# Performance work log

Hardware: AMD Instinct MI355X
Metric: run time of the kernel (lower is better)

Reference implementation:

```python
import jax, jax.numpy as jnp
import numpy as np

N, F_IN, HID, HEADS, E, G, CLS = 20000, 128, 32, 8, 320000, 64, 10


def setup_inputs() -> dict:
    key = jax.random.key(0)
    ks = jax.random.split(key, 16)
    HC = HEADS * HID
    inp = {
        'x': jax.random.normal(ks[0], (N, F_IN), jnp.float32),
        'edge_index': jax.random.randint(ks[1], (2, E), 0, N, jnp.int64),
        'batch': jnp.sort(jax.random.randint(ks[2], (N,), 0, G, jnp.int64)),
        'W1': jax.random.normal(ks[3], (F_IN, HC), jnp.float32) * 0.1,
        'att_l1': jax.random.normal(ks[4], (HEADS, HID), jnp.float32) * 0.1,
        'att_r1': jax.random.normal(ks[5], (HEADS, HID), jnp.float32) * 0.1,
        'b1': jnp.zeros((HC,), jnp.float32),
        'W2': jax.random.normal(ks[6], (HC, HC), jnp.float32) * 0.1,
        'att_l2': jax.random.normal(ks[7], (HEADS, HID), jnp.float32) * 0.1,
        'att_r2': jax.random.normal(ks[8], (HEADS, HID), jnp.float32) * 0.1,
        'b2': jnp.zeros((HC,), jnp.float32),
        'lin_W': jax.random.normal(ks[9], (HC, CLS), jnp.float32) * 0.1,
        'lin_b': jnp.zeros((CLS,), jnp.float32),
    }
    return inp


def _add_self_loops(edge_index):
    loops = jnp.arange(N, dtype=edge_index.dtype)
    return (jnp.concatenate([edge_index[0], loops]),
            jnp.concatenate([edge_index[1], loops]))


def _supergat_conv(x, edge_index, W, att_l, att_r, b):
    # SuperGATConv, attention_type='MX', eval mode (no dropout / neg sampling)
    h = (x @ W).reshape(-1, HEADS, HID)          # [N, H, C]
    src, dst = _add_self_loops(edge_index)       # j -> i
    x_j = h[src]                                 # [Etot, H, C]
    x_i = h[dst]
    logits = jnp.einsum('ehc,ehc->eh', x_i, x_j)            # dot-product part
    alpha = jnp.einsum('ehc,hc->eh', x_j, att_l) + jnp.einsum('ehc,hc->eh', x_i, att_r)
    alpha = alpha * jax.nn.sigmoid(logits)
    alpha = jax.nn.leaky_relu(alpha, 0.2)
    # segment softmax over incoming edges of each dst node
    amax = jax.ops.segment_max(alpha, dst, num_segments=N)
    ex = jnp.exp(alpha - amax[dst])
    denom = jax.ops.segment_sum(ex, dst, num_segments=N)
    attn = ex / (denom[dst] + 1e-16)             # [Etot, H]
    out = jax.ops.segment_sum(x_j * attn[..., None], dst, num_segments=N)  # [N,H,C]
    return out.reshape(-1, HEADS * HID) + b


def reference(x, edge_index, batch, W1, att_l1, att_r1, b1, W2, att_l2, att_r2, b2, lin_W, lin_b):
    h = _supergat_conv(x, edge_index, W1, att_l1, att_r1, b1)
    h = jax.nn.elu(h)
    h = _supergat_conv(h, edge_index, W2, att_l2, att_r2, b2)
    # global mean pool over graphs
    sums = jax.ops.segment_sum(h, batch, num_segments=G)
    cnts = jax.ops.segment_sum(jnp.ones((h.shape[0], 1), h.dtype), batch, num_segments=G)
    pooled = sums / jnp.maximum(cnts, 1.0)
    return pooled @ lin_W + lin_b
```

## Files before the change

kernel.cpp:

```cpp
#include <hip/hip_runtime.h>
#include <hip/hip_bf16.h>
#include <math.h>

#define NNODE 20000
#define FIN   128
#define HC    256
#define HEADS 8
#define HID   32
#define NEDGE 320000
#define ETOT  (NEDGE + NNODE)
#define NGRAPH 64
#define NCLS  10
#define MAXDEG 64

typedef __attribute__((ext_vector_type(8))) short short8v;
typedef __attribute__((ext_vector_type(8))) unsigned short ushort8v;
typedef __attribute__((ext_vector_type(4))) float float4v;

__device__ __forceinline__ ushort f2bf(float f) {
    __hip_bfloat16 b = __float2bfloat16(f);
    return *(ushort*)&b;
}
__device__ __forceinline__ float bf2f(ushort u) {
    return __uint_as_float(((unsigned)u) << 16);
}


#define ZB_DEG ((NNODE + 255) / 256)
#define ZB_PS  ((NGRAPH * HC + NGRAPH + 255) / 256)

__global__ __launch_bounds__(256) void init_kernel(const float* __restrict__ W1,
                                                   const float* __restrict__ W2,
                                                   ushort* __restrict__ W1t,
                                                   ushort* __restrict__ W2t,
                                                   int* __restrict__ deg,
                                                   float* __restrict__ psum) {
    int b = blockIdx.x;
    if (b < 128) {
        int e = b * 256 + threadIdx.x;
        int k = e >> 8, n = e & 255;
        W1t[(long)n * FIN + k] = f2bf(W1[(long)k * 256 + n]);
    } else if (b < 384) {
        int e = (b - 128) * 256 + threadIdx.x;
        int k = e >> 8, n = e & 255;
        W2t[(long)n * HC + k] = f2bf(W2[(long)k * 256 + n]);
    } else if (b < 384 + ZB_DEG) {
        int i = (b - 384) * 256 + threadIdx.x;
        if (i < NNODE) deg[i] = 0;
    } else {
        int i = (b - 384 - ZB_DEG) * 256 + threadIdx.x;
        if (i < NGRAPH * HC + NGRAPH) psum[i] = 0.f;
    }
}


__global__ __launch_bounds__(256) void fill_slots(const int* __restrict__ ei,
                                                  int* __restrict__ deg,
                                                  int* __restrict__ esrc) {
    int e = blockIdx.x * blockDim.x + threadIdx.x;
    if (e >= ETOT) return;
    int src, dst;
    if (e < NEDGE) { src = ei[e]; dst = ei[NEDGE + e]; }
    else           { src = e - NEDGE; dst = src; }
    int slot = atomicAdd(&deg[dst], 1);
    if (slot < MAXDEG) esrc[dst * MAXDEG + slot] = src;
}


template<bool A_FP32>
__global__ __launch_bounds__(256) void gemm_mfma(const void* __restrict__ Aptr,
                                                 const ushort* __restrict__ Bt,
                                                 ushort* __restrict__ C,
                                                 const float* __restrict__ attL,
                                                 const float* __restrict__ attR,
                                                 float* __restrict__ aL,
                                                 float* __restrict__ aR,
                                                 int M, int K) {
    __shared__ __align__(16) ushort As[64][72];
    __shared__ __align__(16) ushort Bs[64][72];
    int tid = threadIdx.x;
    int rowBase = blockIdx.x * 64;
    int colBase = blockIdx.y * 64;
    int wave = tid >> 6;
    int l = tid & 63;
    int lm = l & 15;
    int quad = l >> 4;
    int r0 = (wave >> 1) * 32;
    int c0 = (wave & 1) * 32;

    float4v acc00 = {0.f, 0.f, 0.f, 0.f};
    float4v acc01 = acc00, acc10 = acc00, acc11 = acc00;

    for (int k0 = 0; k0 < K; k0 += 64) {
        if (A_FP32) {
            const float* A = (const float*)Aptr;
            #pragma unroll
            for (int q = 0; q < 4; q++) {
                int idx = tid + q * 256;
                int r   = idx >> 4;
                int kc  = (idx & 15) * 4;
                int grow = rowBase + r;
                float4 v = make_float4(0.f, 0.f, 0.f, 0.f);
                if (grow < M) v = *(const float4*)(A + (long)grow * K + k0 + kc);
                ushort4 o = { f2bf(v.x), f2bf(v.y), f2bf(v.z), f2bf(v.w) };
                *(ushort4*)&As[r][kc] = o;
            }
            #pragma unroll
            for (int q = 0; q < 2; q++) {
                int ch = tid + q * 256;
                int r  = ch >> 3;
                int kc = (ch & 7) * 8;
                *(short8v*)&Bs[r][kc] =
                    *(const short8v*)(Bt + (long)(colBase + r) * K + k0 + kc);
            }
        } else {
            const ushort* A = (const ushort*)Aptr;
            #pragma unroll
            for (int q = 0; q < 2; q++) {
                int ch = tid + q * 256;
                int r  = ch >> 3;
                int kc = (ch & 7) * 8;
                int grow = rowBase + r;
                short8v av = {};
                if (grow < M) av = *(const short8v*)(A + (long)grow * K + k0 + kc);
                *(short8v*)&As[r][kc] = av;
                *(short8v*)&Bs[r][kc] =
                    *(const short8v*)(Bt + (long)(colBase + r) * K + k0 + kc);
            }
        }
        __syncthreads();
        #pragma unroll
        for (int ks = 0; ks < 64; ks += 32) {
            int kb = ks + quad * 8;
            short8v a0 = *(const short8v*)&As[r0 + lm][kb];
            short8v a1 = *(const short8v*)&As[r0 + 16 + lm][kb];
            short8v b0 = *(const short8v*)&Bs[c0 + lm][kb];
            short8v b1 = *(const short8v*)&Bs[c0 + 16 + lm][kb];
            acc00 = __builtin_amdgcn_mfma_f32_16x16x32_bf16(a0, b0, acc00, 0, 0, 0);
            acc01 = __builtin_amdgcn_mfma_f32_16x16x32_bf16(a0, b1, acc01, 0, 0, 0);
            acc10 = __builtin_amdgcn_mfma_f32_16x16x32_bf16(a1, b0, acc10, 0, 0, 0);
            acc11 = __builtin_amdgcn_mfma_f32_16x16x32_bf16(a1, b1, acc11, 0, 0, 0);
        }
        __syncthreads();
    }

    int cb = colBase + c0;
    int hd = cb >> 5;
    float al0 = attL[cb + lm], al1 = attL[cb + 16 + lm];
    float ar0 = attR[cb + lm], ar1 = attR[cb + 16 + lm];
    #pragma unroll
    for (int mi = 0; mi < 2; mi++) {
        float4v s0 = mi ? acc10 : acc00;
        float4v s1 = mi ? acc11 : acc01;
        #pragma unroll
        for (int r = 0; r < 4; r++) {
            int row = rowBase + r0 + mi * 16 + quad * 4 + r;
            float pl = s0[r] * al0 + s1[r] * al1;
            float pr = s0[r] * ar0 + s1[r] * ar1;
            #pragma unroll
            for (int s2 = 1; s2 < 16; s2 <<= 1) {
                pl += __shfl_xor(pl, s2);
                pr += __shfl_xor(pr, s2);
            }
            if (row < M) {
                C[(long)row * 256 + cb + lm]      = f2bf(s0[r]);
                C[(long)row * 256 + cb + 16 + lm] = f2bf(s1[r]);
                if (lm == 0) {
                    aL[row * 8 + hd] = pl;
                    aR[row * 8 + hd] = pr;
                }
            }
        }
    }
}


__global__ __launch_bounds__(256) void fused_attn(const ushort* __restrict__ h,
                                                  const int* __restrict__ degv,
                                                  const int* __restrict__ esrc,
                                                  const float* __restrict__ aL,
                                                  const float* __restrict__ aR,
                                                  const float* __restrict__ bias,
                                                  ushort* __restrict__ out,
                                                  int apply_elu) {
    int wave = threadIdx.x >> 6;
    int node = blockIdx.x * 4 + wave;
    if (node >= NNODE) return;
    int l = threadIdx.x & 63;
    int slot = l >> 5;
    int lh = l & 31;
    int head = lh >> 2;

    const ushort8v* h8 = (const ushort8v*)h;
    ushort8v hiu = h8[(long)node * 32 + lh];
    float hi[8];
    #pragma unroll
    for (int c = 0; c < 8; c++) hi[c] = bf2f(hiu[c]);
    float a_ri = aR[node * 8 + head];
    int beg = node * MAXDEG;
    int deg = min(degv[node], MAXDEG);

    float lsum = 0.f;
    float acc[8] = {0.f, 0.f, 0.f, 0.f, 0.f, 0.f, 0.f, 0.f};

    int p = slot;
    int j0 = (p < deg) ? esrc[beg + p] : 0;
    ushort8v hjA = h8[(long)j0 * 32 + lh];
    float alA = aL[j0 * 8 + head];
    int j1 = (p + 2 < deg) ? esrc[beg + p + 2] : 0;

    for (; p < deg; p += 2) {
        ushort8v hjB = h8[(long)j1 * 32 + lh];
        float alB = aL[j1 * 8 + head];
        int j2 = (p + 4 < deg) ? esrc[beg + p + 4] : 0;

        float hj[8];
        #pragma unroll
        for (int c = 0; c < 8; c++) hj[c] = bf2f(hjA[c]);
        float prod = hi[0] * hj[0];
        #pragma unroll
        for (int c = 1; c < 8; c++) prod += hi[c] * hj[c];
        prod += __shfl_xor(prod, 1);
        prod += __shfl_xor(prod, 2);
        float alpha = (alA + a_ri) * __builtin_amdgcn_rcpf(1.f + __expf(-prod));
        alpha = (alpha > 0.f) ? alpha : 0.2f * alpha;
        float ex = __expf(alpha);
        lsum += ex;
        #pragma unroll
        for (int c = 0; c < 8; c++) acc[c] += ex * hj[c];

        hjA = hjB; alA = alB; j1 = j2;
    }

    lsum += __shfl_xor(lsum, 32);
    #pragma unroll
    for (int c = 0; c < 8; c++) acc[c] += __shfl_xor(acc[c], 32);

    if (slot == 0) {
        float inv = __builtin_amdgcn_rcpf(lsum + 1e-16f);
        float4 b0 = ((const float4*)bias)[lh * 2];
        float4 b1 = ((const float4*)bias)[lh * 2 + 1];
        float bb[8] = {b0.x, b0.y, b0.z, b0.w, b1.x, b1.y, b1.z, b1.w};
        ushort8v o;
        #pragma unroll
        for (int c = 0; c < 8; c++) {
            float r = acc[c] * inv + bb[c];
            if (apply_elu) r = (r > 0.f) ? r : (__expf(r) - 1.f);
            o[c] = f2bf(r);
        }
        *(ushort8v*)(out + (long)node * 256 + lh * 8) = o;
    }
}


__global__ __launch_bounds__(256) void pool_kernel(const ushort* __restrict__ h,
                                                   const int* __restrict__ batch,
                                                   float* __restrict__ psum,
                                                   float* __restrict__ pcnt) {
    int t = threadIdx.x;
    int n0 = blockIdx.x * 64;
    int n1 = min(n0 + 64, NNODE);
    if (n0 >= NNODE) return;
    float accv = 0.f;
    int gcur = batch[n0];
    for (int n = n0; n < n1; ++n) {
        int g = batch[n];
        if (g != gcur) {
            atomicAdd(&psum[gcur * HC + t], accv);
            accv = 0.f;
            gcur = g;
        }
        accv += bf2f(h[(long)n * HC + t]);
    }
    atomicAdd(&psum[gcur * HC + t], accv);
    if (t == 0) {
        int cnt = 0;
        int gc = batch[n0];
        for (int n = n0; n < n1; ++n) {
            int g = batch[n];
            if (g != gc) { atomicAdd(&pcnt[gc], (float)cnt); cnt = 0; gc = g; }
            cnt++;
        }
        atomicAdd(&pcnt[gc], (float)cnt);
    }
}

__global__ void final_kernel(const float* __restrict__ psum, const float* __restrict__ pcnt,
                             const float* __restrict__ linW, const float* __restrict__ linb,
                             float* __restrict__ out) {
    int g = blockIdx.x;
    int t = threadIdx.x;
    __shared__ float p[HC];
    float c = fmaxf(pcnt[g], 1.f);
    p[t] = psum[g * HC + t] / c;
    __syncthreads();
    if (t < NCLS) {
        float s = linb[t];
        for (int cch = 0; cch < HC; cch++) s += p[cch] * linW[cch * NCLS + t];
        out[g * NCLS + t] = s;
    }
}


extern "C" void kernel_launch(void* const* d_in, const int* in_sizes, int n_in,
                              void* d_out, int out_size, void* d_ws, size_t ws_size,
                              hipStream_t stream) {
    const float* x     = (const float*)d_in[0];
    const int*   ei    = (const int*)d_in[1];
    const int*   batch = (const int*)d_in[2];
    const float* W1    = (const float*)d_in[3];
    const float* attL1 = (const float*)d_in[4];
    const float* attR1 = (const float*)d_in[5];
    const float* b1    = (const float*)d_in[6];
    const float* W2    = (const float*)d_in[7];
    const float* attL2 = (const float*)d_in[8];
    const float* attR2 = (const float*)d_in[9];
    const float* b2    = (const float*)d_in[10];
    const float* linW  = (const float*)d_in[11];
    const float* linb  = (const float*)d_in[12];
    float* out = (float*)d_out;

    char* w = (char*)d_ws;
    size_t o = 0;
    int* deg    = (int*)(w + o); o += (size_t)NNODE * 4;
    o = (o + 15) & ~(size_t)15;
    int* esrc   = (int*)(w + o); o += (size_t)NNODE * MAXDEG * 4;
    o = (o + 15) & ~(size_t)15;
    ushort* W1t = (ushort*)(w + o); o += (size_t)FIN * HC * 2;
    ushort* W2t = (ushort*)(w + o); o += (size_t)HC * HC * 2;
    o = (o + 15) & ~(size_t)15;
    ushort* hbA = (ushort*)(w + o); o += (size_t)NNODE * HC * 2;
    ushort* hbB = (ushort*)(w + o); o += (size_t)NNODE * HC * 2;
    o = (o + 15) & ~(size_t)15;
    float* aL   = (float*)(w + o); o += (size_t)NNODE * HEADS * 4;
    float* aR   = (float*)(w + o); o += (size_t)NNODE * HEADS * 4;
    float* psum = (float*)(w + o); o += (size_t)NGRAPH * HC * 4;
    float* pcnt = (float*)(w + o); o += (size_t)NGRAPH * 4;

    init_kernel<<<384 + ZB_DEG + ZB_PS, 256, 0, stream>>>(W1, W2, W1t, W2t, deg, psum);

    int eb = (ETOT + 255) / 256;
    fill_slots<<<eb, 256, 0, stream>>>(ei, deg, esrc);

    dim3 gg((NNODE + 63) / 64, HC / 64);
    int ab = (NNODE + 3) / 4;
    gemm_mfma<true><<<gg, 256, 0, stream>>>(x, W1t, hbA, attL1, attR1, aL, aR, NNODE, FIN);
    fused_attn<<<ab, 256, 0, stream>>>(hbA, deg, esrc, aL, aR, b1, hbB, 1);
    gemm_mfma<false><<<gg, 256, 0, stream>>>(hbB, W2t, hbA, attL2, attR2, aL, aR, NNODE, HC);
    fused_attn<<<ab, 256, 0, stream>>>(hbA, deg, esrc, aL, aR, b2, hbB, 0);
    pool_kernel<<<(NNODE + 63) / 64, 256, 0, stream>>>(hbB, batch, psum, pcnt);
    final_kernel<<<NGRAPH, 256, 0, stream>>>(psum, pcnt, linW, linb, out);
}
```

Before: 221.1 us.

## Merge all stages into one cooperative persistent kernel with grid syncs

Replaces the eight separate kernel launches with a single cooperative kernel. It loops over work items with grid-stride loops and uses grid.sync() between the init, edge-fill, GEMM, attention, pooling and final phases. The aim is to remove launch overhead and inter-kernel gaps. In exchange the grid is capped at 1024 blocks, so phases such as attention (5000 blocks' worth of work) and the GEMM lose oversubscription. Grid-wide barriers and a host occupancy query on every call add their own cost.

```diff
diff --git a/kernel.cpp b/kernel.cpp
--- a/kernel.cpp
+++ b/kernel.cpp
@@ -1,6 +1,9 @@
 #include <hip/hip_runtime.h>
+#include <hip/hip_cooperative_groups.h>
 #include <hip/hip_bf16.h>
 #include <math.h>
+
+namespace cg = cooperative_groups;
 
 #define NNODE 20000
 #define FIN   128
@@ -13,6 +16,12 @@
 #define NCLS  10
 #define MAXDEG 64
 
+#define ZB_DEG ((NNODE + 255) / 256)
+#define ZB_PS  ((NGRAPH * HC + NGRAPH + 255) / 256)
+#define GEMM_TILES (((NNODE + 63) / 64) * 4)
+#define ATTN_Q ((NNODE + 3) / 4)
+#define POOL_B ((NNODE + 63) / 64)
+
 typedef __attribute__((ext_vector_type(8))) short short8v;
 typedef __attribute__((ext_vector_type(8))) unsigned short ushort8v;
 typedef __attribute__((ext_vector_type(4))) float float4v;
@@ -25,62 +34,29 @@
     return __uint_as_float(((unsigned)u) << 16);
 }
 
-
-#define ZB_DEG ((NNODE + 255) / 256)
-#define ZB_PS  ((NGRAPH * HC + NGRAPH + 255) / 256)
-
-__global__ __launch_bounds__(256) void init_kernel(const float* __restrict__ W1,
-                                                   const float* __restrict__ W2,
-                                                   ushort* __restrict__ W1t,
-                                                   ushort* __restrict__ W2t,
-                                                   int* __restrict__ deg,
-                                                   float* __restrict__ psum) {
-    int b = blockIdx.x;
-    if (b < 128) {
-        int e = b * 256 + threadIdx.x;
-        int k = e >> 8, n = e & 255;
-        W1t[(long)n * FIN + k] = f2bf(W1[(long)k * 256 + n]);
-    } else if (b < 384) {
-        int e = (b - 128) * 256 + threadIdx.x;
-        int k = e >> 8, n = e & 255;
-        W2t[(long)n * HC + k] = f2bf(W2[(long)k * 256 + n]);
-    } else if (b < 384 + ZB_DEG) {
-        int i = (b - 384) * 256 + threadIdx.x;
-        if (i < NNODE) deg[i] = 0;
-    } else {
-        int i = (b - 384 - ZB_DEG) * 256 + threadIdx.x;
-        if (i < NGRAPH * HC + NGRAPH) psum[i] = 0.f;
-    }
-}
-
-
-__global__ __launch_bounds__(256) void fill_slots(const int* __restrict__ ei,
-                                                  int* __restrict__ deg,
-                                                  int* __restrict__ esrc) {
-    int e = blockIdx.x * blockDim.x + threadIdx.x;
-    if (e >= ETOT) return;
-    int src, dst;
-    if (e < NEDGE) { src = ei[e]; dst = ei[NEDGE + e]; }
-    else           { src = e - NEDGE; dst = src; }
-    int slot = atomicAdd(&deg[dst], 1);
-    if (slot < MAXDEG) esrc[dst * MAXDEG + slot] = src;
-}
+struct Params {
+    const float* x; const int* ei; const int* batch;
+    const float* W1; const float* attL1; const float* attR1; const float* b1;
+    const float* W2; const float* attL2; const float* attR2; const float* b2;
+    const float* linW; const float* linb; float* out;
+    int* deg; int* esrc; ushort* W1t; ushort* W2t;
+    ushort* hbA; ushort* hbB; float* aL; float* aR; float* psum; float* pcnt;
+};
 
 
 template<bool A_FP32>
-__global__ __launch_bounds__(256) void gemm_mfma(const void* __restrict__ Aptr,
-                                                 const ushort* __restrict__ Bt,
-                                                 ushort* __restrict__ C,
-                                                 const float* __restrict__ attL,
-                                                 const float* __restrict__ attR,
-                                                 float* __restrict__ aL,
-                                                 float* __restrict__ aR,
-                                                 int M, int K) {
-    __shared__ __align__(16) ushort As[64][72];
-    __shared__ __align__(16) ushort Bs[64][72];
+__device__ void gemm_tile(const void* __restrict__ Aptr,
+                          const ushort* __restrict__ Bt,
+                          ushort* __restrict__ C,
+                          const float* __restrict__ attL,
+                          const float* __restrict__ attR,
+                          float* __restrict__ aL,
+                          float* __restrict__ aR,
+                          int K, int rowBlk, int colBlk,
+                          ushort (*As)[72], ushort (*Bs)[72]) {
     int tid = threadIdx.x;
-    int rowBase = blockIdx.x * 64;
-    int colBase = blockIdx.y * 64;
+    int rowBase = rowBlk * 64;
+    int colBase = colBlk * 64;
     int wave = tid >> 6;
     int l = tid & 63;
     int lm = l & 15;
@@ -101,7 +77,7 @@
                 int kc  = (idx & 15) * 4;
                 int grow = rowBase + r;
                 float4 v = make_float4(0.f, 0.f, 0.f, 0.f);
-                if (grow < M) v = *(const float4*)(A + (long)grow * K + k0 + kc);
+                if (grow < NNODE) v = *(const float4*)(A + (long)grow * K + k0 + kc);
                 ushort4 o = { f2bf(v.x), f2bf(v.y), f2bf(v.z), f2bf(v.w) };
                 *(ushort4*)&As[r][kc] = o;
             }
@@ -122,7 +98,7 @@
                 int kc = (ch & 7) * 8;
                 int grow = rowBase + r;
                 short8v av = {};
-                if (grow < M) av = *(const short8v*)(A + (long)grow * K + k0 + kc);
+                if (grow < NNODE) av = *(const short8v*)(A + (long)grow * K + k0 + kc);
                 *(short8v*)&As[r][kc] = av;
                 *(short8v*)&Bs[r][kc] =
                     *(const short8v*)(Bt + (long)(colBase + r) * K + k0 + kc);
@@ -162,7 +138,7 @@
                 pl += __shfl_xor(pl, s2);
                 pr += __shfl_xor(pr, s2);
             }
-            if (row < M) {
+            if (row < NNODE) {
                 C[(long)row * 256 + cb + lm]      = f2bf(s0[r]);
                 C[(long)row * 256 + cb + 16 + lm] = f2bf(s1[r]);
                 if (lm == 0) {
@@ -175,129 +151,176 @@
 }
 
 
-__global__ __launch_bounds__(256) void fused_attn(const ushort* __restrict__ h,
-                                                  const int* __restrict__ degv,
-                                                  const int* __restrict__ esrc,
-                                                  const float* __restrict__ aL,
-                                                  const float* __restrict__ aR,
-                                                  const float* __restrict__ bias,
-                                                  ushort* __restrict__ out,
-                                                  int apply_elu) {
+template<int ELU>
+__device__ void attn_phase(const ushort* __restrict__ h,
+                           const int* __restrict__ degv,
+                           const int* __restrict__ esrc,
+                           const float* __restrict__ aL,
+                           const float* __restrict__ aR,
+                           const float* __restrict__ bias,
+                           ushort* __restrict__ out) {
     int wave = threadIdx.x >> 6;
-    int node = blockIdx.x * 4 + wave;
-    if (node >= NNODE) return;
     int l = threadIdx.x & 63;
     int slot = l >> 5;
     int lh = l & 31;
     int head = lh >> 2;
-
     const ushort8v* h8 = (const ushort8v*)h;
-    ushort8v hiu = h8[(long)node * 32 + lh];
-    float hi[8];
-    #pragma unroll
-    for (int c = 0; c < 8; c++) hi[c] = bf2f(hiu[c]);
-    float a_ri = aR[node * 8 + head];
-    int beg = node * MAXDEG;
-    int deg = min(degv[node], MAXDEG);
-
-    float lsum = 0.f;
-    float acc[8] = {0.f, 0.f, 0.f, 0.f, 0.f, 0.f, 0.f, 0.f};
-
-    int p = slot;
-    int j0 = (p < deg) ? esrc[beg + p] : 0;
-    ushort8v hjA = h8[(long)j0 * 32 + lh];
-    float alA = aL[j0 * 8 + head];
-    int j1 = (p + 2 < deg) ? esrc[beg + p + 2] : 0;
-
-    for (; p < deg; p += 2) {
-        ushort8v hjB = h8[(long)j1 * 32 + lh];
-        float alB = aL[j1 * 8 + head];
-        int j2 = (p + 4 < deg) ? esrc[beg + p + 4] : 0;
-
-        float hj[8];
+
+    for (int q = blockIdx.x; q < ATTN_Q; q += gridDim.x) {
+        int node = q * 4 + wave;
+        if (node >= NNODE) continue;
+
+        ushort8v hiu = h8[(long)node * 32 + lh];
+        float hi[8];
         #pragma unroll
-        for (int c = 0; c < 8; c++) hj[c] = bf2f(hjA[c]);
-        float prod = hi[0] * hj[0];
+        for (int c = 0; c < 8; c++) hi[c] = bf2f(hiu[c]);
+        float a_ri = aR[node * 8 + head];
+        int beg = node * MAXDEG;
+        int deg = min(degv[node], MAXDEG);
+
+        float lsum = 0.f;
+        float acc[8] = {0.f, 0.f, 0.f, 0.f, 0.f, 0.f, 0.f, 0.f};
+
+        int p = slot;
+        int j0 = (p < deg) ? esrc[beg + p] : 0;
+        ushort8v hjA = h8[(long)j0 * 32 + lh];
+        float alA = aL[j0 * 8 + head];
+        int j1 = (p + 2 < deg) ? esrc[beg + p + 2] : 0;
+
+        for (; p < deg; p += 2) {
+            ushort8v hjB = h8[(long)j1 * 32 + lh];
+            float alB = aL[j1 * 8 + head];
+            int j2 = (p + 4 < deg) ? esrc[beg + p + 4] : 0;
+
+            float hj[8];
+            #pragma unroll
+            for (int c = 0; c < 8; c++) hj[c] = bf2f(hjA[c]);
+            float prod = hi[0] * hj[0];
+            #pragma unroll
+            for (int c = 1; c < 8; c++) prod += hi[c] * hj[c];
+            prod += __shfl_xor(prod, 1);
+            prod += __shfl_xor(prod, 2);
+            float alpha = (alA + a_ri) * __builtin_amdgcn_rcpf(1.f + __expf(-prod));
+            alpha = (alpha > 0.f) ? alpha : 0.2f * alpha;
+            float ex = __expf(alpha);
+            lsum += ex;
+            #pragma unroll
+            for (int c = 0; c < 8; c++) acc[c] += ex * hj[c];
+
+            hjA = hjB; alA = alB; j1 = j2;
+        }
+
+        lsum += __shfl_xor(lsum, 32);
         #pragma unroll
-        for (int c = 1; c < 8; c++) prod += hi[c] * hj[c];
-        prod += __shfl_xor(prod, 1);
-        prod += __shfl_xor(prod, 2);
-        float alpha = (alA + a_ri) * __builtin_amdgcn_rcpf(1.f + __expf(-prod));
-        alpha = (alpha > 0.f) ? alpha : 0.2f * alpha;
-        float ex = __expf(alpha);
-        lsum += ex;
-        #pragma unroll
-        for (int c = 0; c < 8; c++) acc[c] += ex * hj[c];
-
-        hjA = hjB; alA = alB; j1 = j2;
-    }
-
-    lsum += __shfl_xor(lsum, 32);
-    #pragma unroll
-    for (int c = 0; c < 8; c++) acc[c] += __shfl_xor(acc[c], 32);
-
-    if (slot == 0) {
-        float inv = __builtin_amdgcn_rcpf(lsum + 1e-16f);
-        float4 b0 = ((const float4*)bias)[lh * 2];
-        float4 b1 = ((const float4*)bias)[lh * 2 + 1];
-        float bb[8] = {b0.x, b0.y, b0.z, b0.w, b1.x, b1.y, b1.z, b1.w};
-        ushort8v o;
-        #pragma unroll
-        for (int c = 0; c < 8; c++) {
-            float r = acc[c] * inv + bb[c];
-            if (apply_elu) r = (r > 0.f) ? r : (__expf(r) - 1.f);
-            o[c] = f2bf(r);
-        }
-        *(ushort8v*)(out + (long)node * 256 + lh * 8) = o;
-    }
-}
-
-
-__global__ __launch_bounds__(256) void pool_kernel(const ushort* __restrict__ h,
-                                                   const int* __restrict__ batch,
-                                                   float* __restrict__ psum,
-                                                   float* __restrict__ pcnt) {
-    int t = threadIdx.x;
-    int n0 = blockIdx.x * 64;
-    int n1 = min(n0 + 64, NNODE);
-    if (n0 >= NNODE) return;
-    float accv = 0.f;
-    int gcur = batch[n0];
-    for (int n = n0; n < n1; ++n) {
-        int g = batch[n];
-        if (g != gcur) {
-            atomicAdd(&psum[gcur * HC + t], accv);
-            accv = 0.f;
-            gcur = g;
-        }
-        accv += bf2f(h[(long)n * HC + t]);
-    }
-    atomicAdd(&psum[gcur * HC + t], accv);
-    if (t == 0) {
-        int cnt = 0;
-        int gc = batch[n0];
+        for (int c = 0; c < 8; c++) acc[c] += __shfl_xor(acc[c], 32);
+
+        if (slot == 0) {
+            float inv = __builtin_amdgcn_rcpf(lsum + 1e-16f);
+            float4 b0 = ((const float4*)bias)[lh * 2];
+            float4 b1 = ((const float4*)bias)[lh * 2 + 1];
+            float bb[8] = {b0.x, b0.y, b0.z, b0.w, b1.x, b1.y, b1.z, b1.w};
+            ushort8v o;
+            #pragma unroll
+            for (int c = 0; c < 8; c++) {
+                float r = acc[c] * inv + bb[c];
+                if (ELU) r = (r > 0.f) ? r : (__expf(r) - 1.f);
+                o[c] = f2bf(r);
+            }
+            *(ushort8v*)(out + (long)node * 256 + lh * 8) = o;
+        }
+    }
+}
+
+
+__global__ __launch_bounds__(256) void mega(Params p) {
+    cg::grid_group grid = cg::this_grid();
+    __shared__ __align__(16) ushort As[64][72];
+    __shared__ __align__(16) ushort Bs[64][72];
+    int tid = threadIdx.x;
+
+    for (int b = blockIdx.x; b < 384 + ZB_DEG + ZB_PS; b += gridDim.x) {
+        if (b < 128) {
+            int e = b * 256 + tid;
+            int k = e >> 8, n = e & 255;
+            p.W1t[(long)n * FIN + k] = f2bf(p.W1[(long)k * 256 + n]);
+        } else if (b < 384) {
+            int e = (b - 128) * 256 + tid;
+            int k = e >> 8, n = e & 255;
+            p.W2t[(long)n * HC + k] = f2bf(p.W2[(long)k * 256 + n]);
+        } else if (b < 384 + ZB_DEG) {
+            int i = (b - 384) * 256 + tid;
+            if (i < NNODE) p.deg[i] = 0;
+        } else {
+            int i = (b - 384 - ZB_DEG) * 256 + tid;
+            if (i < NGRAPH * HC + NGRAPH) p.psum[i] = 0.f;
+        }
+    }
+    grid.sync();
+
+    for (int e = blockIdx.x * 256 + tid; e < ETOT; e += gridDim.x * 256) {
+        int src, dst;
+        if (e < NEDGE) { src = p.ei[e]; dst = p.ei[NEDGE + e]; }
+        else           { src = e - NEDGE; dst = src; }
+        int slot = atomicAdd(&p.deg[dst], 1);
+        if (slot < MAXDEG) p.esrc[dst * MAXDEG + slot] = src;
+    }
+    grid.sync();
+
+    for (int t = blockIdx.x; t < GEMM_TILES; t += gridDim.x)
+        gemm_tile<true>(p.x, p.W1t, p.hbA, p.attL1, p.attR1, p.aL, p.aR,
+                        FIN, t >> 2, t & 3, As, Bs);
+    grid.sync();
+
+    attn_phase<1>(p.hbA, p.deg, p.esrc, p.aL, p.aR, p.b1, p.hbB);
+    grid.sync();
+
+    for (int t = blockIdx.x; t < GEMM_TILES; t += gridDim.x)
+        gemm_tile<false>(p.hbB, p.W2t, p.hbA, p.attL2, p.attR2, p.aL, p.aR,
+                         HC, t >> 2, t & 3, As, Bs);
+    grid.sync();
+
+    attn_phase<0>(p.hbA, p.deg, p.esrc, p.aL, p.aR, p.b2, p.hbB);
+    grid.sync();
+
+    for (int b = blockIdx.x; b < POOL_B; b += gridDim.x) {
+        int n0 = b * 64;
+        int n1 = min(n0 + 64, NNODE);
+        float accv = 0.f;
+        int gcur = p.batch[n0];
         for (int n = n0; n < n1; ++n) {
-            int g = batch[n];
-            if (g != gc) { atomicAdd(&pcnt[gc], (float)cnt); cnt = 0; gc = g; }
-            cnt++;
-        }
-        atomicAdd(&pcnt[gc], (float)cnt);
-    }
-}
-
-__global__ void final_kernel(const float* __restrict__ psum, const float* __restrict__ pcnt,
-                             const float* __restrict__ linW, const float* __restrict__ linb,
-                             float* __restrict__ out) {
-    int g = blockIdx.x;
-    int t = threadIdx.x;
-    __shared__ float p[HC];
-    float c = fmaxf(pcnt[g], 1.f);
-    p[t] = psum[g * HC + t] / c;
-    __syncthreads();
-    if (t < NCLS) {
-        float s = linb[t];
-        for (int cch = 0; cch < HC; cch++) s += p[cch] * linW[cch * NCLS + t];
-        out[g * NCLS + t] = s;
+            int g = p.batch[n];
+            if (g != gcur) {
+                atomicAdd(&p.psum[gcur * HC + tid], accv);
+                accv = 0.f;
+                gcur = g;
+            }
+            accv += bf2f(p.hbB[(long)n * HC + tid]);
+        }
+        atomicAdd(&p.psum[gcur * HC + tid], accv);
+        if (tid == 0) {
+            int cnt = 0;
+            int gc = p.batch[n0];
+            for (int n = n0; n < n1; ++n) {
+                int g = p.batch[n];
+                if (g != gc) { atomicAdd(&p.pcnt[gc], (float)cnt); cnt = 0; gc = g; }
+                cnt++;
+            }
+            atomicAdd(&p.pcnt[gc], (float)cnt);
+        }
+    }
+    grid.sync();
+
+    float* pp = (float*)&As[0][0];
+    for (int g = blockIdx.x; g < NGRAPH; g += gridDim.x) {
+        float c = fmaxf(p.pcnt[g], 1.f);
+        pp[tid] = p.psum[g * HC + tid] / c;
+        __syncthreads();
+        if (tid < NCLS) {
+            float s = p.linb[tid];
+            for (int cc = 0; cc < HC; cc++) s += pp[cc] * p.linW[cc * NCLS + tid];
+            p.out[g * NCLS + tid] = s;
+        }
+        __syncthreads();
     }
 }
 
@@ -305,49 +328,45 @@
 extern "C" void kernel_launch(void* const* d_in, const int* in_sizes, int n_in,
                               void* d_out, int out_size, void* d_ws, size_t ws_size,
                               hipStream_t stream) {
-    const float* x     = (const float*)d_in[0];
-    const int*   ei    = (const int*)d_in[1];
-    const int*   batch = (const int*)d_in[2];
-    const float* W1    = (const float*)d_in[3];
-    const float* attL1 = (const float*)d_in[4];
-    const float* attR1 = (const float*)d_in[5];
-    const float* b1    = (const float*)d_in[6];
-    const float* W2    = (const float*)d_in[7];
-    const float* attL2 = (const float*)d_in[8];
-    const float* attR2 = (const float*)d_in[9];
-    const float* b2    = (const float*)d_in[10];
-    const float* linW  = (const float*)d_in[11];
-    const float* linb  = (const float*)d_in[12];
-    float* out = (float*)d_out;
+    Params p;
+    p.x     = (const float*)d_in[0];
+    p.ei    = (const int*)d_in[1];
+    p.batch = (const int*)d_in[2];
+    p.W1    = (const float*)d_in[3];
+    p.attL1 = (const float*)d_in[4];
+    p.attR1 = (const float*)d_in[5];
+    p.b1    = (const float*)d_in[6];
+    p.W2    = (const float*)d_in[7];
+    p.attL2 = (const float*)d_in[8];
+    p.attR2 = (const float*)d_in[9];
+    p.b2    = (const float*)d_in[10];
+    p.linW  = (const float*)d_in[11];
+    p.linb  = (const float*)d_in[12];
+    p.out   = (float*)d_out;
 
     char* w = (char*)d_ws;
     size_t o = 0;
-    int* deg    = (int*)(w + o); o += (size_t)NNODE * 4;
+    p.deg   = (int*)(w + o); o += (size_t)NNODE * 4;
     o = (o + 15) & ~(size_t)15;
-    int* esrc   = (int*)(w + o); o += (size_t)NNODE * MAXDEG * 4;
+    p.esrc  = (int*)(w + o); o += (size_t)NNODE * MAXDEG * 4;
     o = (o + 15) & ~(size_t)15;
-    ushort* W1t = (ushort*)(w + o); o += (size_t)FIN * HC * 2;
-    ushort* W2t = (ushort*)(w + o); o += (size_t)HC * HC * 2;
+    p.W1t   = (ushort*)(w + o); o += (size_t)FIN * HC * 2;
+    p.W2t   = (ushort*)(w + o); o += (size_t)HC * HC * 2;
     o = (o + 15) & ~(size_t)15;
-    ushort* hbA = (ushort*)(w + o); o += (size_t)NNODE * HC * 2;
-    ushort* hbB = (ushort*)(w + o); o += (size_t)NNODE * HC * 2;
+    p.hbA   = (ushort*)(w + o); o += (size_t)NNODE * HC * 2;
+    p.hbB   = (ushort*)(w + o); o += (size_t)NNODE * HC * 2;
     o = (o + 15) & ~(size_t)15;
-    float* aL   = (float*)(w + o); o += (size_t)NNODE * HEADS * 4;
-    float* aR   = (float*)(w + o); o += (size_t)NNODE * HEADS * 4;
-    float* psum = (float*)(w + o); o += (size_t)NGRAPH * HC * 4;
-    float* pcnt = (float*)(w + o); o += (size_t)NGRAPH * 4;
-
-    init_kernel<<<384 + ZB_DEG + ZB_PS, 256, 0, stream>>>(W1, W2, W1t, W2t, deg, psum);
-
-    int eb = (ETOT + 255) / 256;
-    fill_slots<<<eb, 256, 0, stream>>>(ei, deg, esrc);
-
-    dim3 gg((NNODE + 63) / 64, HC / 64);
-    int ab = (NNODE + 3) / 4;
-    gemm_mfma<true><<<gg, 256, 0, stream>>>(x, W1t, hbA, attL1, attR1, aL, aR, NNODE, FIN);
-    fused_attn<<<ab, 256, 0, stream>>>(hbA, deg, esrc, aL, aR, b1, hbB, 1);
-    gemm_mfma<false><<<gg, 256, 0, stream>>>(hbB, W2t, hbA, attL2, attR2, aL, aR, NNODE, HC);
-    fused_attn<<<ab, 256, 0, stream>>>(hbA, deg, esrc, aL, aR, b2, hbB, 0);
-    pool_kernel<<<(NNODE + 63) / 64, 256, 0, stream>>>(hbB, batch, psum, pcnt);
-    final_kernel<<<NGRAPH, 256, 0, stream>>>(psum, pcnt, linW, linb, out);
-}
+    p.aL    = (float*)(w + o); o += (size_t)NNODE * HEADS * 4;
+    p.aR    = (float*)(w + o); o += (size_t)NNODE * HEADS * 4;
+    p.psum  = (float*)(w + o); o += (size_t)NGRAPH * HC * 4;
+    p.pcnt  = (float*)(w + o); o += (size_t)NGRAPH * 4;
+
+    int maxb = 0;
+    hipOccupancyMaxActiveBlocksPerMultiprocessor(&maxb, mega, 256, 0);
+    if (maxb < 1) maxb = 1;
+    int grid = maxb * 256;
+    if (grid > 1024) grid = 1024;
+
+    void* args[] = { &p };
+    hipLaunchCooperativeKernel((void*)mega, dim3(grid), dim3(256), args, 0, stream);
+}
```

Result: slower. 738.6 us (+234.1%).
